# Performance work log

Hardware: AMD Instinct MI355X
Metric: run time of the kernel (lower is better)

The kernel has to match this reference:

```python
import jax, jax.numpy as jnp
import numpy as np

B, S, D = 2, 2048, 7168
R, H, VD = 1024, 16, 128
QK_HD = R // H            # 64, per-head latent q/k dim
SCALE = float(np.sqrt(D // H))  # self.scale = d_heads ** 0.5 = sqrt(448)


def setup_inputs() -> dict:
    key = jax.random.key(0)
    ks = jax.random.split(key, 6)
    return {
        "x":   jax.random.normal(ks[0], (B, S, D), dtype=jnp.float32),
        "Wq":  jax.random.normal(ks[1], (R, D), dtype=jnp.float32) * 0.02,
        "Wkv": jax.random.normal(ks[2], (R, D), dtype=jnp.float32) * 0.02,
        "Wvb": jax.random.normal(ks[3], (H * VD, R), dtype=jnp.float32) * 0.02,
        "Wo":  jax.random.normal(ks[4], (D, H * VD), dtype=jnp.float32) * 0.02,
        "bo":  jnp.zeros((D,), dtype=jnp.float32),
    }


def reference(x, Wq, Wkv, Wvb, Wo, bo):
    b, s, d = x.shape
    # low-rank compressed projections (torch Linear: y = x @ W.T)
    q_lat  = x @ Wq.T            # [B,S,R] compressed query
    kv_lat = x @ Wkv.T           # [B,S,R] compressed KV latent (shared K)
    q = q_lat.reshape(b, s, H, QK_HD)    # [B,S,H,64]
    k = kv_lat.reshape(b, s, H, QK_HD)   # [B,S,H,64]
    # up-project values from latent
    v = (kv_lat @ Wvb.T).reshape(b, s, H, VD)  # [B,S,H,128]
    # scaled causal attention in latent head space
    scores = jnp.einsum("bqhd,bkhd->bhqk", q, k) / SCALE  # [B,H,S,S]
    causal = jnp.tril(jnp.ones((s, s), dtype=bool))
    scores = jnp.where(causal, scores, jnp.finfo(scores.dtype).min)
    attn = jax.nn.softmax(scores, axis=-1)
    out = jnp.einsum("bhqk,bkhd->bqhd", attn, v).reshape(b, s, H * VD)
    return out @ Wo.T + bo       # [B,S,D]
```

## Files before the change

### kernel.cpp

```cpp
#include <hip/hip_runtime.h>
#include <hip/hip_bf16.h>

typedef __bf16 bf16_t;
typedef __attribute__((ext_vector_type(8))) __bf16 bf16x8;
typedef __attribute__((ext_vector_type(4))) __bf16 bf16x4;
typedef __attribute__((ext_vector_type(4))) float f32x4;

#define B_ 2
#define S_ 2048
#define D_ 7168
#define R_ 1024
#define H_ 16
#define VD_ 128
#define MROWS 4096
#define NQKV 2048
#define HVD 2048

__device__ __forceinline__ void gload_lds16(const bf16_t* g, bf16_t* l) {
    __builtin_amdgcn_global_load_lds(
        (const __attribute__((address_space(1))) unsigned int*)(g),
        (__attribute__((address_space(3))) unsigned int*)(l),
        16, 0, 0);
}

__global__ __launch_bounds__(256)
void cvt_f32_bf16(const float* __restrict__ src, bf16_t* __restrict__ dst, float scale) {
    size_t i = ((size_t)blockIdx.x * 256 + threadIdx.x) * 4;
    f32x4 v = *(const f32x4*)(src + i);
    bf16x4 o;
    o[0] = (bf16_t)(v[0] * scale);
    o[1] = (bf16_t)(v[1] * scale);
    o[2] = (bf16_t)(v[2] * scale);
    o[3] = (bf16_t)(v[3] * scale);
    *(bf16x4*)(dst + i) = o;
}

template<int OUTF32>
__global__ __launch_bounds__(256)
void gemm_bt(const bf16_t* __restrict__ A, int lda,
             const bf16_t* __restrict__ Bt, int ldb,
             void* __restrict__ Cv, int ldc,
             const float* __restrict__ bias, int K)
{
    __shared__ __align__(16) bf16_t As[128 * 64];
    __shared__ __align__(16) bf16_t Bs[128 * 64];
    const int tid  = threadIdx.x;
    const int lane = tid & 63;
    const int wave = tid >> 6;
    const int tileM = blockIdx.y * 128;
    const int tileN = blockIdx.x * 128;
    const int wr = (wave >> 1) * 64;
    const int wc = (wave & 1) * 64;
    const int r  = lane & 15;
    const int kq = lane >> 4;

    const bf16_t* Ag = A  + (size_t)tileM * lda;
    const bf16_t* Bg = Bt + (size_t)tileN * ldb;

    f32x4 acc[4][4] = {};

    for (int k0 = 0; k0 < K; k0 += 64) {
        #pragma unroll
        for (int i = 0; i < 4; ++i) {
            const int lin  = (i * 256 + tid) * 8;
            const int arow = lin >> 6;
            const int acol = (lin & 63) ^ ((arow & 7) << 3);
            gload_lds16(Ag + (size_t)arow * lda + k0 + acol, As + lin);
            gload_lds16(Bg + (size_t)arow * ldb + k0 + acol, Bs + lin);
        }
        __syncthreads();

        bf16x8 af[4][2], bfr[4][2];
        #pragma unroll
        for (int m = 0; m < 4; ++m)
            #pragma unroll
            for (int kk = 0; kk < 2; ++kk) {
                const int e = (wr + m * 16 + r) * 64 + kk * 32 + kq * 8;
                af[m][kk] = *(const bf16x8*)(As + (e ^ ((r & 7) << 3)));
            }
        #pragma unroll
        for (int n = 0; n < 4; ++n)
            #pragma unroll
            for (int kk = 0; kk < 2; ++kk) {
                const int e = (wc + n * 16 + r) * 64 + kk * 32 + kq * 8;
                bfr[n][kk] = *(const bf16x8*)(Bs + (e ^ ((r & 7) << 3)));
            }
        #pragma unroll
        for (int kk = 0; kk < 2; ++kk)
            #pragma unroll
            for (int m = 0; m < 4; ++m)
                #pragma unroll
                for (int n = 0; n < 4; ++n)
                    acc[m][n] = __builtin_amdgcn_mfma_f32_16x16x32_bf16(af[m][kk], bfr[n][kk], acc[m][n], 0, 0, 0);
        __syncthreads();
    }

    const int orow = tileM + wr + kq * 4;
    const int ocol = tileN + wc + r;
    if (OUTF32) {
        float* C = (float*)Cv;
        #pragma unroll
        for (int n = 0; n < 4; ++n) {
            float bv = bias[ocol + n * 16];
            #pragma unroll
            for (int m = 0; m < 4; ++m)
                #pragma unroll
                for (int j = 0; j < 4; ++j)
                    C[(size_t)(orow + m * 16 + j) * ldc + ocol + n * 16] = acc[m][n][j] + bv;
        }
    } else {
        bf16_t* C = (bf16_t*)Cv;
        #pragma unroll
        for (int m = 0; m < 4; ++m)
            #pragma unroll
            for (int n = 0; n < 4; ++n)
                #pragma unroll
                for (int j = 0; j < 4; ++j)
                    C[(size_t)(orow + m * 16 + j) * ldc + ocol + n * 16] = (bf16_t)acc[m][n][j];
    }
}

__device__ __forceinline__ void attn_qtile(
    const bf16_t* __restrict__ Q, const bf16_t* __restrict__ Kp,
    const bf16_t* __restrict__ Vp, bf16_t* __restrict__ Op,
    bf16_t* __restrict__ P_lds, int qbase, int lane)
{
    const int r  = lane & 15;
    const int kq = lane >> 4;

    bf16x8 qf[2][2];
    #pragma unroll
    for (int m = 0; m < 2; ++m)
        #pragma unroll
        for (int kk = 0; kk < 2; ++kk)
            qf[m][kk] = *(const bf16x8*)(Q + (size_t)(qbase + m * 16 + r) * NQKV + kk * 32 + kq * 8);

    f32x4 o[2][8] = {};
    float mst[2][4], lst[2][4];
    #pragma unroll
    for (int m = 0; m < 2; ++m)
        #pragma unroll
        for (int j = 0; j < 4; ++j) { mst[m][j] = -INFINITY; lst[m][j] = 0.0f; }

    const int nfull  = qbase >> 6;
    const int ntiles = (qbase + 95) >> 6;

    for (int t = 0; t < ntiles; ++t) {
        const int kvb = t * 64;
        f32x4 s[2][4] = {};
        #pragma unroll
        for (int n = 0; n < 4; ++n) {
            bf16x8 kf0 = *(const bf16x8*)(Kp + (size_t)(kvb + n * 16 + r) * NQKV + kq * 8);
            bf16x8 kf1 = *(const bf16x8*)(Kp + (size_t)(kvb + n * 16 + r) * NQKV + 32 + kq * 8);
            #pragma unroll
            for (int m = 0; m < 2; ++m) {
                s[m][n] = __builtin_amdgcn_mfma_f32_16x16x32_bf16(qf[m][0], kf0, s[m][n], 0, 0, 0);
                s[m][n] = __builtin_amdgcn_mfma_f32_16x16x32_bf16(qf[m][1], kf1, s[m][n], 0, 0, 0);
            }
        }
        if (t >= nfull) {
            #pragma unroll
            for (int m = 0; m < 2; ++m)
                #pragma unroll
                for (int n = 0; n < 4; ++n)
                    #pragma unroll
                    for (int j = 0; j < 4; ++j) {
                        int kc = kvb + n * 16 + r;
                        int qr = qbase + m * 16 + kq * 4 + j;
                        if (kc > qr) s[m][n][j] = -1e30f;
                    }
        }
        float mx[2][4];
        #pragma unroll
        for (int m = 0; m < 2; ++m)
            #pragma unroll
            for (int j = 0; j < 4; ++j) {
                float v = fmaxf(fmaxf(s[m][0][j], s[m][1][j]), fmaxf(s[m][2][j], s[m][3][j]));
                #pragma unroll
                for (int d = 1; d < 16; d <<= 1) v = fmaxf(v, __shfl_xor(v, d, 64));
                mx[m][j] = v;
            }
        bool need = false;
        #pragma unroll
        for (int m = 0; m < 2; ++m)
            #pragma unroll
            for (int j = 0; j < 4; ++j) need |= (mx[m][j] > mst[m][j] + 8.0f);
        if (__ballot(need)) {
            #pragma unroll
            for (int m = 0; m < 2; ++m)
                #pragma unroll
                for (int j = 0; j < 4; ++j) {
                    float mnew  = fmaxf(mst[m][j], mx[m][j]);
                    float alpha = __expf(mst[m][j] - mnew);
                    lst[m][j] *= alpha;
                    mst[m][j]  = mnew;
                    #pragma unroll
                    for (int n = 0; n < 8; ++n) o[m][n][j] *= alpha;
                }
        }
        #pragma unroll
        for (int m = 0; m < 2; ++m)
            #pragma unroll
            for (int j = 0; j < 4; ++j) {
                float rs = 0.0f;
                const int row = m * 16 + kq * 4 + j;
                #pragma unroll
                for (int n = 0; n < 4; ++n) {
                    float pv = __expf(s[m][n][j] - mst[m][j]);
                    rs += pv;
                    const int c = (n * 16 + r) ^ ((row & 7) << 3);
                    P_lds[row * 64 + c] = (bf16_t)pv;
                }
                #pragma unroll
                for (int d = 1; d < 16; d <<= 1) rs += __shfl_xor(rs, d, 64);
                lst[m][j] += rs;
            }
        __syncthreads();
        bf16x8 pf[2][2];
        #pragma unroll
        for (int m = 0; m < 2; ++m)
            #pragma unroll
            for (int kk = 0; kk < 2; ++kk) {
                const int e = (m * 16 + r) * 64 + kk * 32 + kq * 8;
                pf[m][kk] = *(const bf16x8*)(P_lds + (e ^ ((r & 7) << 3)));
            }
        #pragma unroll
        for (int n = 0; n < 8; ++n) {
            #pragma unroll
            for (int kk = 0; kk < 2; ++kk) {
                bf16x8 vf = *(const bf16x8*)(Vp + (size_t)(n * 16 + r) * MROWS + kvb + kk * 32 + kq * 8);
                #pragma unroll
                for (int m = 0; m < 2; ++m)
                    o[m][n] = __builtin_amdgcn_mfma_f32_16x16x32_bf16(pf[m][kk], vf, o[m][n], 0, 0, 0);
            }
        }
        __syncthreads();
    }

    #pragma unroll
    for (int m = 0; m < 2; ++m)
        #pragma unroll
        for (int j = 0; j < 4; ++j) {
            float inv = 1.0f / lst[m][j];
            int row = m * 16 + kq * 4 + j;
            #pragma unroll
            for (int n = 0; n < 8; ++n)
                Op[(size_t)(qbase + row) * HVD + n * 16 + r] = (bf16_t)(o[m][n][j] * inv);
        }
}

__global__ __launch_bounds__(64)
void attn_kernel(const bf16_t* __restrict__ qkv, const bf16_t* __restrict__ Vt,
                 bf16_t* __restrict__ O)
{
    __shared__ __align__(16) bf16_t P_lds[32 * 64];
    const int lane = threadIdx.x;
    const int p = blockIdx.x;
    const int h = blockIdx.y;
    const int b = blockIdx.z;

    const bf16_t* Q  = qkv + (size_t)(b * S_) * NQKV + h * 64;
    const bf16_t* Kp = qkv + (size_t)(b * S_) * NQKV + R_ + h * 64;
    const bf16_t* Vp = Vt + (size_t)(h * VD_) * MROWS + b * S_;
    bf16_t* Op = O + (size_t)(b * S_) * HVD + h * VD_;

    attn_qtile(Q, Kp, Vp, Op, P_lds, (63 - p) * 32, lane);
    attn_qtile(Q, Kp, Vp, Op, P_lds, p * 32, lane);
}

extern "C" void kernel_launch(void* const* d_in, const int* in_sizes, int n_in,
                              void* d_out, int out_size, void* d_ws, size_t ws_size,
                              hipStream_t stream) {
    const float* x   = (const float*)d_in[0];
    const float* Wq  = (const float*)d_in[1];
    const float* Wkv = (const float*)d_in[2];
    const float* Wvb = (const float*)d_in[3];
    const float* Wo  = (const float*)d_in[4];
    const float* bo  = (const float*)d_in[5];

    char* oc = (char*)d_out;
    bf16_t* xb     = (bf16_t*)oc;
    bf16_t* Wqkv_b = (bf16_t*)(oc + 58720256);
    char* ws = (char*)d_ws;
    bf16_t* qkv_b  = (bf16_t*)ws;
    bf16_t* Wvb_b  = (bf16_t*)(ws + 16777216);
    bf16_t* Vt_b   = (bf16_t*)(ws + 20971520);
    bf16_t* attn_b = (bf16_t*)(ws + 37748736);
    bf16_t* Wo_b   = (bf16_t*)(ws + 54525952);

    const float inv_scale = 0.047245559f;

    cvt_f32_bf16<<<29360128 / 1024, 256, 0, stream>>>(x,   xb, 1.0f);
    cvt_f32_bf16<<< 7340032 / 1024, 256, 0, stream>>>(Wq,  Wqkv_b, inv_scale);
    cvt_f32_bf16<<< 7340032 / 1024, 256, 0, stream>>>(Wkv, Wqkv_b + 7340032, 1.0f);
    cvt_f32_bf16<<< 2097152 / 1024, 256, 0, stream>>>(Wvb, Wvb_b, 1.0f);
    cvt_f32_bf16<<<14680064 / 1024, 256, 0, stream>>>(Wo,  Wo_b, 1.0f);

    gemm_bt<0><<<dim3(16, 32), 256, 0, stream>>>(xb, D_, Wqkv_b, D_, qkv_b, NQKV, nullptr, D_);
    gemm_bt<0><<<dim3(32, 16), 256, 0, stream>>>(Wvb_b, R_, qkv_b + R_, NQKV, Vt_b, MROWS, nullptr, R_);
    attn_kernel<<<dim3(32, H_, B_), 64, 0, stream>>>(qkv_b, Vt_b, attn_b);
    gemm_bt<1><<<dim3(56, 32), 256, 0, stream>>>(attn_b, HVD, Wo_b, HVD, d_out, D_, bo, HVD);
}
```

Measured before the change: 542.0 us.

## Double-buffer GEMM LDS tiles and shrink attention q-tile to 16 rows

The GEMM now keeps two LDS buffers and prefetches the tile two steps ahead, using explicit vmcnt waits and barriers, so global loads overlap the MFMA work. Separately, the attention kernel processes 16-row query tiles instead of 32, doubling the grid to 64x16x2 single-wave blocks for more parallelism and fewer wasted causal tiles. The trade-offs are double the GEMM LDS use, which may lower occupancy, and halved K/V reuse per attention wave, which means more global K/V traffic.

```diff
diff --git a/kernel.cpp b/kernel.cpp
--- a/kernel.cpp
+++ b/kernel.cpp
@@ -42,8 +42,8 @@
              void* __restrict__ Cv, int ldc,
              const float* __restrict__ bias, int K)
 {
-    __shared__ __align__(16) bf16_t As[128 * 64];
-    __shared__ __align__(16) bf16_t Bs[128 * 64];
+    __shared__ __align__(16) bf16_t As[2][128 * 64];
+    __shared__ __align__(16) bf16_t Bs[2][128 * 64];
     const int tid  = threadIdx.x;
     const int lane = tid & 63;
     const int wave = tid >> 6;
@@ -57,18 +57,36 @@
     const bf16_t* Ag = A  + (size_t)tileM * lda;
     const bf16_t* Bg = Bt + (size_t)tileN * ldb;
 
+    int srow[4], scol[4], slin[4];
+    #pragma unroll
+    for (int i = 0; i < 4; ++i) {
+        slin[i] = (i * 256 + tid) * 8;
+        srow[i] = slin[i] >> 6;
+        scol[i] = (slin[i] & 63) ^ ((srow[i] & 7) << 3);
+    }
+
+    #define ISSUE_TILE(buf, k0)                                                  \
+        {                                                                        \
+            _Pragma("unroll")                                                    \
+            for (int i = 0; i < 4; ++i) {                                        \
+                gload_lds16(Ag + (size_t)srow[i] * lda + (k0) + scol[i], As[buf] + slin[i]); \
+                gload_lds16(Bg + (size_t)srow[i] * ldb + (k0) + scol[i], Bs[buf] + slin[i]); \
+            }                                                                    \
+        }
+
     f32x4 acc[4][4] = {};
-
-    for (int k0 = 0; k0 < K; k0 += 64) {
-        #pragma unroll
-        for (int i = 0; i < 4; ++i) {
-            const int lin  = (i * 256 + tid) * 8;
-            const int arow = lin >> 6;
-            const int acol = (lin & 63) ^ ((arow & 7) << 3);
-            gload_lds16(Ag + (size_t)arow * lda + k0 + acol, As + lin);
-            gload_lds16(Bg + (size_t)arow * ldb + k0 + acol, Bs + lin);
-        }
-        __syncthreads();
+    const int nt = K >> 6;
+
+    ISSUE_TILE(0, 0)
+    ISSUE_TILE(1, 64)
+    asm volatile("s_waitcnt vmcnt(8)" ::: "memory");
+    __builtin_amdgcn_s_barrier();
+    __builtin_amdgcn_sched_barrier(0);
+
+    for (int t = 0; t < nt; ++t) {
+        const int cur = t & 1;
+        const bf16_t* Ab = As[cur];
+        const bf16_t* Bb = Bs[cur];
 
         bf16x8 af[4][2], bfr[4][2];
         #pragma unroll
@@ -76,14 +94,14 @@
             #pragma unroll
             for (int kk = 0; kk < 2; ++kk) {
                 const int e = (wr + m * 16 + r) * 64 + kk * 32 + kq * 8;
-                af[m][kk] = *(const bf16x8*)(As + (e ^ ((r & 7) << 3)));
+                af[m][kk] = *(const bf16x8*)(Ab + (e ^ ((r & 7) << 3)));
             }
         #pragma unroll
         for (int n = 0; n < 4; ++n)
             #pragma unroll
             for (int kk = 0; kk < 2; ++kk) {
                 const int e = (wc + n * 16 + r) * 64 + kk * 32 + kq * 8;
-                bfr[n][kk] = *(const bf16x8*)(Bs + (e ^ ((r & 7) << 3)));
+                bfr[n][kk] = *(const bf16x8*)(Bb + (e ^ ((r & 7) << 3)));
             }
         #pragma unroll
         for (int kk = 0; kk < 2; ++kk)
@@ -92,8 +110,19 @@
                 #pragma unroll
                 for (int n = 0; n < 4; ++n)
                     acc[m][n] = __builtin_amdgcn_mfma_f32_16x16x32_bf16(af[m][kk], bfr[n][kk], acc[m][n], 0, 0, 0);
-        __syncthreads();
-    }
+
+        __builtin_amdgcn_s_barrier();
+        __builtin_amdgcn_sched_barrier(0);
+        if (t + 2 < nt) {
+            ISSUE_TILE(cur, (t + 2) << 6)
+            asm volatile("s_waitcnt vmcnt(8)" ::: "memory");
+        } else {
+            asm volatile("s_waitcnt vmcnt(0)" ::: "memory");
+        }
+        __builtin_amdgcn_s_barrier();
+        __builtin_amdgcn_sched_barrier(0);
+    }
+    #undef ISSUE_TILE
 
     const int orow = tileM + wr + kq * 4;
     const int ocol = tileN + wc + r;
@@ -120,7 +149,7 @@
     }
 }
 
-__device__ __forceinline__ void attn_qtile(
+__device__ __forceinline__ void attn_qtile16(
     const bf16_t* __restrict__ Q, const bf16_t* __restrict__ Kp,
     const bf16_t* __restrict__ Vp, bf16_t* __restrict__ Op,
     bf16_t* __restrict__ P_lds, int qbase, int lane)
@@ -128,132 +157,109 @@
     const int r  = lane & 15;
     const int kq = lane >> 4;
 
-    bf16x8 qf[2][2];
+    bf16x8 qf[2];
     #pragma unroll
-    for (int m = 0; m < 2; ++m)
-        #pragma unroll
-        for (int kk = 0; kk < 2; ++kk)
-            qf[m][kk] = *(const bf16x8*)(Q + (size_t)(qbase + m * 16 + r) * NQKV + kk * 32 + kq * 8);
-
-    f32x4 o[2][8] = {};
-    float mst[2][4], lst[2][4];
+    for (int kk = 0; kk < 2; ++kk)
+        qf[kk] = *(const bf16x8*)(Q + (size_t)(qbase + r) * NQKV + kk * 32 + kq * 8);
+
+    f32x4 o[8] = {};
+    float mst[4], lst[4];
     #pragma unroll
-    for (int m = 0; m < 2; ++m)
-        #pragma unroll
-        for (int j = 0; j < 4; ++j) { mst[m][j] = -INFINITY; lst[m][j] = 0.0f; }
+    for (int j = 0; j < 4; ++j) { mst[j] = -INFINITY; lst[j] = 0.0f; }
 
     const int nfull  = qbase >> 6;
-    const int ntiles = (qbase + 95) >> 6;
+    const int ntiles = (qbase + 79) >> 6;
 
     for (int t = 0; t < ntiles; ++t) {
         const int kvb = t * 64;
-        f32x4 s[2][4] = {};
+        f32x4 s[4] = {};
         #pragma unroll
         for (int n = 0; n < 4; ++n) {
             bf16x8 kf0 = *(const bf16x8*)(Kp + (size_t)(kvb + n * 16 + r) * NQKV + kq * 8);
             bf16x8 kf1 = *(const bf16x8*)(Kp + (size_t)(kvb + n * 16 + r) * NQKV + 32 + kq * 8);
-            #pragma unroll
-            for (int m = 0; m < 2; ++m) {
-                s[m][n] = __builtin_amdgcn_mfma_f32_16x16x32_bf16(qf[m][0], kf0, s[m][n], 0, 0, 0);
-                s[m][n] = __builtin_amdgcn_mfma_f32_16x16x32_bf16(qf[m][1], kf1, s[m][n], 0, 0, 0);
-            }
+            s[n] = __builtin_amdgcn_mfma_f32_16x16x32_bf16(qf[0], kf0, s[n], 0, 0, 0);
+            s[n] = __builtin_amdgcn_mfma_f32_16x16x32_bf16(qf[1], kf1, s[n], 0, 0, 0);
         }
         if (t >= nfull) {
             #pragma unroll
-            for (int m = 0; m < 2; ++m)
-                #pragma unroll
-                for (int n = 0; n < 4; ++n)
-                    #pragma unroll
-                    for (int j = 0; j < 4; ++j) {
-                        int kc = kvb + n * 16 + r;
-                        int qr = qbase + m * 16 + kq * 4 + j;
-                        if (kc > qr) s[m][n][j] = -1e30f;
-                    }
-        }
-        float mx[2][4];
-        #pragma unroll
-        for (int m = 0; m < 2; ++m)
+            for (int n = 0; n < 4; ++n)
+                #pragma unroll
+                for (int j = 0; j < 4; ++j) {
+                    int kc = kvb + n * 16 + r;
+                    int qr = qbase + kq * 4 + j;
+                    if (kc > qr) s[n][j] = -1e30f;
+                }
+        }
+        float mx[4];
+        #pragma unroll
+        for (int j = 0; j < 4; ++j) {
+            float v = fmaxf(fmaxf(s[0][j], s[1][j]), fmaxf(s[2][j], s[3][j]));
+            #pragma unroll
+            for (int d = 1; d < 16; d <<= 1) v = fmaxf(v, __shfl_xor(v, d, 64));
+            mx[j] = v;
+        }
+        bool need = false;
+        #pragma unroll
+        for (int j = 0; j < 4; ++j) need |= (mx[j] > mst[j] + 8.0f);
+        if (__ballot(need)) {
             #pragma unroll
             for (int j = 0; j < 4; ++j) {
-                float v = fmaxf(fmaxf(s[m][0][j], s[m][1][j]), fmaxf(s[m][2][j], s[m][3][j]));
-                #pragma unroll
-                for (int d = 1; d < 16; d <<= 1) v = fmaxf(v, __shfl_xor(v, d, 64));
-                mx[m][j] = v;
-            }
-        bool need = false;
-        #pragma unroll
-        for (int m = 0; m < 2; ++m)
-            #pragma unroll
-            for (int j = 0; j < 4; ++j) need |= (mx[m][j] > mst[m][j] + 8.0f);
-        if (__ballot(need)) {
-            #pragma unroll
-            for (int m = 0; m < 2; ++m)
-                #pragma unroll
-                for (int j = 0; j < 4; ++j) {
-                    float mnew  = fmaxf(mst[m][j], mx[m][j]);
-                    float alpha = __expf(mst[m][j] - mnew);
-                    lst[m][j] *= alpha;
-                    mst[m][j]  = mnew;
-                    #pragma unroll
-                    for (int n = 0; n < 8; ++n) o[m][n][j] *= alpha;
-                }
-        }
-        #pragma unroll
-        for (int m = 0; m < 2; ++m)
-            #pragma unroll
-            for (int j = 0; j < 4; ++j) {
-                float rs = 0.0f;
-                const int row = m * 16 + kq * 4 + j;
-                #pragma unroll
-                for (int n = 0; n < 4; ++n) {
-                    float pv = __expf(s[m][n][j] - mst[m][j]);
-                    rs += pv;
-                    const int c = (n * 16 + r) ^ ((row & 7) << 3);
-                    P_lds[row * 64 + c] = (bf16_t)pv;
-                }
-                #pragma unroll
-                for (int d = 1; d < 16; d <<= 1) rs += __shfl_xor(rs, d, 64);
-                lst[m][j] += rs;
-            }
+                float mnew  = fmaxf(mst[j], mx[j]);
+                float alpha = __expf(mst[j] - mnew);
+                lst[j] *= alpha;
+                mst[j]  = mnew;
+                #pragma unroll
+                for (int n = 0; n < 8; ++n) o[n][j] *= alpha;
+            }
+        }
+        #pragma unroll
+        for (int j = 0; j < 4; ++j) {
+            float rs = 0.0f;
+            const int row = kq * 4 + j;
+            #pragma unroll
+            for (int n = 0; n < 4; ++n) {
+                float pv = __expf(s[n][j] - mst[j]);
+                rs += pv;
+                const int c = (n * 16 + r) ^ ((row & 7) << 3);
+                P_lds[row * 64 + c] = (bf16_t)pv;
+            }
+            #pragma unroll
+            for (int d = 1; d < 16; d <<= 1) rs += __shfl_xor(rs, d, 64);
+            lst[j] += rs;
+        }
         __syncthreads();
-        bf16x8 pf[2][2];
-        #pragma unroll
-        for (int m = 0; m < 2; ++m)
-            #pragma unroll
-            for (int kk = 0; kk < 2; ++kk) {
-                const int e = (m * 16 + r) * 64 + kk * 32 + kq * 8;
-                pf[m][kk] = *(const bf16x8*)(P_lds + (e ^ ((r & 7) << 3)));
-            }
+        bf16x8 pf[2];
+        #pragma unroll
+        for (int kk = 0; kk < 2; ++kk) {
+            const int e = r * 64 + kk * 32 + kq * 8;
+            pf[kk] = *(const bf16x8*)(P_lds + (e ^ ((r & 7) << 3)));
+        }
         #pragma unroll
         for (int n = 0; n < 8; ++n) {
             #pragma unroll
             for (int kk = 0; kk < 2; ++kk) {
                 bf16x8 vf = *(const bf16x8*)(Vp + (size_t)(n * 16 + r) * MROWS + kvb + kk * 32 + kq * 8);
-                #pragma unroll
-                for (int m = 0; m < 2; ++m)
-                    o[m][n] = __builtin_amdgcn_mfma_f32_16x16x32_bf16(pf[m][kk], vf, o[m][n], 0, 0, 0);
+                o[n] = __builtin_amdgcn_mfma_f32_16x16x32_bf16(pf[kk], vf, o[n], 0, 0, 0);
             }
         }
         __syncthreads();
     }
 
     #pragma unroll
-    for (int m = 0; m < 2; ++m)
-        #pragma unroll
-        for (int j = 0; j < 4; ++j) {
-            float inv = 1.0f / lst[m][j];
-            int row = m * 16 + kq * 4 + j;
-            #pragma unroll
-            for (int n = 0; n < 8; ++n)
-                Op[(size_t)(qbase + row) * HVD + n * 16 + r] = (bf16_t)(o[m][n][j] * inv);
-        }
+    for (int j = 0; j < 4; ++j) {
+        float inv = 1.0f / lst[j];
+        int row = kq * 4 + j;
+        #pragma unroll
+        for (int n = 0; n < 8; ++n)
+            Op[(size_t)(qbase + row) * HVD + n * 16 + r] = (bf16_t)(o[n][j] * inv);
+    }
 }
 
 __global__ __launch_bounds__(64)
 void attn_kernel(const bf16_t* __restrict__ qkv, const bf16_t* __restrict__ Vt,
                  bf16_t* __restrict__ O)
 {
-    __shared__ __align__(16) bf16_t P_lds[32 * 64];
+    __shared__ __align__(16) bf16_t P_lds[16 * 64];
     const int lane = threadIdx.x;
     const int p = blockIdx.x;
     const int h = blockIdx.y;
@@ -264,8 +270,8 @@
     const bf16_t* Vp = Vt + (size_t)(h * VD_) * MROWS + b * S_;
     bf16_t* Op = O + (size_t)(b * S_) * HVD + h * VD_;
 
-    attn_qtile(Q, Kp, Vp, Op, P_lds, (63 - p) * 32, lane);
-    attn_qtile(Q, Kp, Vp, Op, P_lds, p * 32, lane);
+    attn_qtile16(Q, Kp, Vp, Op, P_lds, (127 - p) * 16, lane);
+    attn_qtile16(Q, Kp, Vp, Op, P_lds, p * 16, lane);
 }
 
 extern "C" void kernel_launch(void* const* d_in, const int* in_sizes, int n_in,
@@ -298,6 +304,6 @@
 
     gemm_bt<0><<<dim3(16, 32), 256, 0, stream>>>(xb, D_, Wqkv_b, D_, qkv_b, NQKV, nullptr, D_);
     gemm_bt<0><<<dim3(32, 16), 256, 0, stream>>>(Wvb_b, R_, qkv_b + R_, NQKV, Vt_b, MROWS, nullptr, R_);
-    attn_kernel<<<dim3(32, H_, B_), 64, 0, stream>>>(qkv_b, Vt_b, attn_b);
+    attn_kernel<<<dim3(64, H_, B_), 64, 0, stream>>>(qkv_b, Vt_b, attn_b);
     gemm_bt<1><<<dim3(56, 32), 256, 0, stream>>>(attn_b, HVD, Wo_b, HVD, d_out, D_, bo, HVD);
 }
```

New measurement: 611.7 us. +12.9%, slower.
